# Optimization experiments

Measured on AMD Instinct MI355X. Metric: run time of the kernel, lower is better.

The kernel has to match this reference:

```python
import jax, jax.numpy as jnp
import numpy as np

# SREChead (single level, width=0.25): stem 1x1 (128->64) + two 3x3 convs (64->64),
# each Conv->BN(eval, folded into scale/shift)->SiLU, then 1x1 reg (4ch) and obj (1ch)
# heads, followed by YOLOX-style grid decode.
B, C_IN, HGT, WID = 64, 128, 80, 80
C_H = 64            # int(256 * 0.25)
STRIDE = 32


def _conv(x, w):
    # NCHW conv, stride 1, SAME padding (pad=(k-1)//2 as in BaseConv)
    return jax.lax.conv_general_dilated(
        x, w, window_strides=(1, 1), padding='SAME',
        dimension_numbers=('NCHW', 'OIHW', 'NCHW'))


def _bn_silu(y, scale, shift):
    # eval-mode BatchNorm folded to per-channel affine, then SiLU
    return jax.nn.silu(y * scale[None, :, None, None] + shift[None, :, None, None])


def setup_inputs() -> dict:
    key = jax.random.key(0)
    ks = jax.random.split(key, 12)

    def w(k, o, i, kh, kw, s=0.05):
        return jax.random.normal(k, (o, i, kh, kw), jnp.float32) * s

    def bn(k, c):
        k1, k2 = jax.random.split(k)
        scale = 1.0 + 0.1 * jax.random.normal(k1, (c,), jnp.float32)
        shift = 0.05 * jax.random.normal(k2, (c,), jnp.float32)
        return scale, shift

    stem_scale, stem_shift = bn(ks[2], C_H)
    c1_scale, c1_shift = bn(ks[4], C_H)
    c2_scale, c2_shift = bn(ks[6], C_H)
    return {
        'x': jax.random.normal(ks[0], (B, C_IN, HGT, WID), jnp.float32),
        'stem_w': w(ks[1], C_H, C_IN, 1, 1),
        'stem_scale': stem_scale, 'stem_shift': stem_shift,
        'c1_w': w(ks[3], C_H, C_H, 3, 3),
        'c1_scale': c1_scale, 'c1_shift': c1_shift,
        'c2_w': w(ks[5], C_H, C_H, 3, 3),
        'c2_scale': c2_scale, 'c2_shift': c2_shift,
        'reg_w': w(ks[7], 4, C_H, 1, 1),
        'reg_b': jnp.zeros((4,), jnp.float32),
        'obj_w': w(ks[8], 1, C_H, 1, 1),
        'obj_b': jnp.zeros((1,), jnp.float32),
    }


def reference(x, stem_w, stem_scale, stem_shift,
              c1_w, c1_scale, c1_shift,
              c2_w, c2_scale, c2_shift,
              reg_w, reg_b, obj_w, obj_b):
    f = _bn_silu(_conv(x, stem_w), stem_scale, stem_shift)       # [B,64,H,W]
    f = _bn_silu(_conv(f, c1_w), c1_scale, c1_shift)
    f = _bn_silu(_conv(f, c2_w), c2_scale, c2_shift)
    reg = _conv(f, reg_w) + reg_b[None, :, None, None]           # [B,4,H,W]
    obj = jax.nn.sigmoid(_conv(f, obj_w) + obj_b[None, :, None, None])  # [B,1,H,W]
    out = jnp.concatenate([reg, obj], axis=1)                    # [B,5,H,W]
    out = out.reshape(out.shape[0], 5, HGT * WID).transpose(0, 2, 1)  # [B,HW,5]
    # YOLOX decode: xy = (pred_xy + grid) * stride, wh = exp(pred_wh) * stride
    yv, xv = jnp.meshgrid(jnp.arange(HGT), jnp.arange(WID), indexing='ij')
    grid = jnp.stack([xv, yv], -1).reshape(1, HGT * WID, 2).astype(out.dtype)
    xy = (out[..., :2] + grid) * STRIDE
    wh = jnp.exp(out[..., 2:4]) * STRIDE
    return jnp.concatenate([xy, wh, out[..., 4:5]], axis=-1)     # [B,HW,5]
```

## Files before the change

### kernel.cpp

```cpp
#include <hip/hip_runtime.h>
#include <cstdint>


typedef short short8 __attribute__((ext_vector_type(8)));
typedef float floatx4 __attribute__((ext_vector_type(4)));
typedef float fx4 __attribute__((ext_vector_type(4)));
typedef unsigned short us4 __attribute__((ext_vector_type(4)));

#define NPIX 6400
#define CGS 3952
#define SGS 1024

static __device__ __forceinline__ unsigned short f2bf(float f) {
    unsigned u = __builtin_bit_cast(unsigned, f);
    u += 0x7fffu + ((u >> 16) & 1u);
    return (unsigned short)(u >> 16);
}

static __device__ __forceinline__ float silu_(float v) {
    return v / (1.0f + __expf(-v));
}

__global__ __launch_bounds__(256) void rearr_w_kernel(
    const float* __restrict__ ws_, const float* __restrict__ w1,
    const float* __restrict__ w2,
    unsigned short* __restrict__ wS, unsigned short* __restrict__ wB1,
    unsigned short* __restrict__ wB2) {
    int idx = blockIdx.x * 256 + threadIdx.x;
    if (idx < 8192) {
        int e = idx;
        int j = e & 7, lane = (e >> 3) & 63, ct = (e >> 9) & 3, kb = e >> 11;
        int co = ct * 16 + (lane & 15);
        int ci = kb * 32 + ((lane >> 4) * 8) + j;
        wS[e] = f2bf(ws_[co * 128 + ci]);
        return;
    }
    idx -= 8192;
    const float* src = (idx < 36864) ? w1 : w2;
    unsigned short* dst = (idx < 36864) ? wB1 : wB2;
    int e = (idx < 36864) ? idx : idx - 36864;
    int j = e & 7, lane = (e >> 3) & 63, ct = (e >> 9) & 3, kb = e >> 11;
    int co = ct * 16 + (lane & 15);
    int k = kb * 32 + ((lane >> 4) * 8) + j;
    int ci = k & 63, tap = k >> 6;
    dst[e] = f2bf(src[(co * 64 + ci) * 9 + tap]);
}

__global__ __launch_bounds__(256) void stem_kernel(
    const float* __restrict__ x, const unsigned short* __restrict__ wS,
    const float* __restrict__ scale, const float* __restrict__ shift,
    unsigned short* __restrict__ f1) {
    __shared__ __align__(16) unsigned short xt[16 * SGS];
    int b = blockIdx.y;
    int tid = threadIdx.x;
    int pbase = blockIdx.x * 128;
    int lane = tid & 63, wv = tid >> 6;
    int l15 = lane & 15, q = lane >> 4;

    #pragma unroll
    for (int k = 0; k < 8; ++k) {
        int item = k * 256 + tid;
        int g = item >> 7, px = item & 127;
        const float* xp = x + ((size_t)b * 128 + g * 8) * NPIX + pbase + px;
        unsigned short tmp[8];
        #pragma unroll
        for (int j = 0; j < 8; ++j) tmp[j] = f2bf(xp[j * NPIX]);
        *(short8*)(xt + g * SGS + px * 8) = *(const short8*)tmp;
    }

    float sc[4][4], sh[4][4];
    #pragma unroll
    for (int ct = 0; ct < 4; ++ct)
        #pragma unroll
        for (int r = 0; r < 4; ++r) {
            sc[ct][r] = scale[ct * 16 + q * 4 + r];
            sh[ct][r] = shift[ct * 16 + q * 4 + r];
        }

    __syncthreads();

    floatx4 acc[4][2];
    floatx4 zf = {0.0f, 0.0f, 0.0f, 0.0f};
    #pragma unroll
    for (int ct = 0; ct < 4; ++ct)
        #pragma unroll
        for (int t = 0; t < 2; ++t) acc[ct][t] = zf;

    #pragma unroll
    for (int kb = 0; kb < 4; ++kb) {
        short8 wf[4];
        #pragma unroll
        for (int ct = 0; ct < 4; ++ct)
            wf[ct] = *(const short8*)(wS + ((kb * 4 + ct) * 64 + lane) * 8);
        short8 xf[2];
        #pragma unroll
        for (int t = 0; t < 2; ++t) {
            int px = (wv * 2 + t) * 16 + l15;
            xf[t] = *(const short8*)(xt + (kb * 4 + q) * SGS + px * 8);
        }
        #pragma unroll
        for (int ct = 0; ct < 4; ++ct)
            #pragma unroll
            for (int t = 0; t < 2; ++t)
                acc[ct][t] = __builtin_amdgcn_mfma_f32_16x16x32_bf16(
                    wf[ct], xf[t], acc[ct][t], 0, 0, 0);
    }

    #pragma unroll
    for (int t = 0; t < 2; ++t) {
        int pg = pbase + (wv * 2 + t) * 16 + l15;
        unsigned short* dst = f1 + ((size_t)b * NPIX + pg) * 64;
        #pragma unroll
        for (int ct = 0; ct < 4; ++ct) {
            us4 v;
            #pragma unroll
            for (int r = 0; r < 4; ++r)
                v[r] = f2bf(silu_(acc[ct][t][r] * sc[ct][r] + sh[ct][r]));
            *(us4*)(dst + ct * 16 + q * 4) = v;
        }
    }
}

static __device__ __forceinline__ void conv_core(
    const unsigned short* __restrict__ fin, const unsigned short* __restrict__ wB,
    unsigned short* tile, floatx4* acc, int b, int y0,
    int tid, int lane, int wv, int l15, int q) {
    const unsigned short* fb = fin + (size_t)b * NPIX * 64;
    #pragma unroll
    for (int i = 0; i < 16; ++i) {
        int cid = i * 256 + tid;
        if (cid < 3936) {
            int pixL = cid >> 3, chunk = cid & 7;
            int r = pixL / 82, c = pixL - r * 82;
            int gy = y0 - 1 + r, gx = c - 1;
            short8 v = {};
            if ((unsigned)gy < 80u && (unsigned)gx < 80u)
                v = *(const short8*)(fb + (size_t)(gy * 80 + gx) * 64 + chunk * 8);
            *(short8*)(tile + chunk * CGS + pixL * 8) = v;
        }
    }

    __syncthreads();

    floatx4 zf = {0.0f, 0.0f, 0.0f, 0.0f};
    #pragma unroll
    for (int pt = 0; pt < 20; ++pt) acc[pt] = zf;

    #pragma unroll
    for (int trow = 0; trow < 3; ++trow) {
        short8 wrow[6];
        #pragma unroll
        for (int i = 0; i < 6; ++i)
            wrow[i] = *(const short8*)(wB + (((trow * 6 + i) * 4 + wv) * 64 + lane) * 8);
        const int dy = trow - 1;
        #pragma unroll
        for (int tc = 0; tc < 3; ++tc) {
            const int dx = tc - 1;
            #pragma unroll
            for (int half = 0; half < 2; ++half) {
                short8 w8 = wrow[tc * 2 + half];
                #pragma unroll
                for (int pt = 0; pt < 20; ++pt) {
                    const int r_o = pt / 5, c_o = (pt % 5) * 16;
                    int pix = (r_o + 1 + dy) * 82 + c_o + l15 + 1 + dx;
                    short8 b8 = *(const short8*)(tile + (half * 4 + q) * CGS + pix * 8);
                    acc[pt] = __builtin_amdgcn_mfma_f32_16x16x32_bf16(
                        w8, b8, acc[pt], 0, 0, 0);
                }
            }
        }
    }
}

__global__ __launch_bounds__(256) void conv3_kernel(
    const unsigned short* __restrict__ fin, const unsigned short* __restrict__ wB,
    const float* __restrict__ scale, const float* __restrict__ shift,
    unsigned short* __restrict__ fout) {
    __shared__ __align__(16) unsigned short tile[8 * CGS];
    int b = blockIdx.y, y0 = blockIdx.x * 4;
    int tid = threadIdx.x;
    int lane = tid & 63, wv = tid >> 6;
    int l15 = lane & 15, q = lane >> 4;

    floatx4 acc[20];
    conv_core(fin, wB, tile, acc, b, y0, tid, lane, wv, l15, q);

    float sc4[4], sh4[4];
    #pragma unroll
    for (int r = 0; r < 4; ++r) {
        sc4[r] = scale[wv * 16 + q * 4 + r];
        sh4[r] = shift[wv * 16 + q * 4 + r];
    }
    #pragma unroll
    for (int pt = 0; pt < 20; ++pt) {
        const int r_o = pt / 5, c_o = (pt % 5) * 16;
        int pg = (y0 + r_o) * 80 + c_o + l15;
        us4 v;
        #pragma unroll
        for (int r = 0; r < 4; ++r)
            v[r] = f2bf(silu_(acc[pt][r] * sc4[r] + sh4[r]));
        *(us4*)(fout + ((size_t)b * NPIX + pg) * 64 + wv * 16 + q * 4) = v;
    }
}

__global__ __launch_bounds__(256) void conv_head_kernel(
    const unsigned short* __restrict__ fin, const unsigned short* __restrict__ wB,
    const float* __restrict__ scale, const float* __restrict__ shift,
    const float* __restrict__ reg_w, const float* __restrict__ reg_b,
    const float* __restrict__ obj_w, const float* __restrict__ obj_b,
    float* __restrict__ out) {
    __shared__ __align__(16) unsigned short tile[8 * CGS];
    int b = blockIdx.y, y0 = blockIdx.x * 4;
    int tid = threadIdx.x;
    int lane = tid & 63, wv = tid >> 6;
    int l15 = lane & 15, q = lane >> 4;

    floatx4 acc[20];
    conv_core(fin, wB, tile, acc, b, y0, tid, lane, wv, l15, q);

    __syncthreads();

    float sc4[4], sh4[4];
    #pragma unroll
    for (int r = 0; r < 4; ++r) {
        sc4[r] = scale[wv * 16 + q * 4 + r];
        sh4[r] = shift[wv * 16 + q * 4 + r];
    }
    int gco = wv * 2 + (q >> 1);
    #pragma unroll
    for (int pt = 0; pt < 20; ++pt) {
        const int r_o = pt / 5, c_o = (pt % 5) * 16;
        int pix = r_o * 80 + c_o + l15;
        us4 v;
        #pragma unroll
        for (int r = 0; r < 4; ++r)
            v[r] = f2bf(silu_(acc[pt][r] * sc4[r] + sh4[r]));
        *(us4*)(tile + gco * CGS + pix * 8 + (q & 1) * 4) = v;
    }

    short8 hbf[2];
    #pragma unroll
    for (int kb2 = 0; kb2 < 2; ++kb2) {
        int k0 = kb2 * 32 + q * 8;
        short8 f = {};
        if (l15 < 4) {
            #pragma unroll
            for (int j = 0; j < 8; ++j) f[j] = (short)f2bf(reg_w[l15 * 64 + k0 + j]);
        } else if (l15 == 4) {
            #pragma unroll
            for (int j = 0; j < 8; ++j) f[j] = (short)f2bf(obj_w[k0 + j]);
        }
        hbf[kb2] = f;
    }

    __syncthreads();

    floatx4 zf = {0.0f, 0.0f, 0.0f, 0.0f};
    floatx4 acc5[5];
    #pragma unroll
    for (int t = 0; t < 5; ++t) acc5[t] = zf;
    #pragma unroll
    for (int t = 0; t < 5; ++t) {
        int mt = wv * 5 + t;
        #pragma unroll
        for (int kb2 = 0; kb2 < 2; ++kb2) {
            int pix = mt * 16 + l15;
            short8 a = *(const short8*)(tile + (kb2 * 4 + q) * CGS + pix * 8);
            acc5[t] = __builtin_amdgcn_mfma_f32_16x16x32_bf16(
                a, hbf[kb2], acc5[t], 0, 0, 0);
        }
    }

    float bias = 0.0f;
    if (l15 < 4) bias = reg_b[l15];
    else if (l15 == 4) bias = obj_b[0];

    #pragma unroll
    for (int t = 0; t < 5; ++t) {
        int mt = wv * 5 + t;
        #pragma unroll
        for (int r = 0; r < 4; ++r) {
            int pixL = mt * 16 + q * 4 + r;
            if (l15 < 5) {
                float v = acc5[t][r] + bias;
                float gx = (float)(pixL % 80);
                float gy = (float)(y0 + pixL / 80);
                float o;
                if (l15 == 0)      o = (v + gx) * 32.0f;
                else if (l15 == 1) o = (v + gy) * 32.0f;
                else if (l15 < 4)  o = __expf(v) * 32.0f;
                else               o = 1.0f / (1.0f + __expf(-v));
                out[((size_t)b * NPIX + y0 * 80 + pixL) * 5 + l15] = o;
            }
        }
    }
}

extern "C" void kernel_launch(void* const* d_in, const int* in_sizes, int n_in,
                              void* d_out, int out_size, void* d_ws, size_t ws_size,
                              hipStream_t stream) {
    const float* x          = (const float*)d_in[0];
    const float* stem_w     = (const float*)d_in[1];
    const float* stem_scale = (const float*)d_in[2];
    const float* stem_shift = (const float*)d_in[3];
    const float* c1_w       = (const float*)d_in[4];
    const float* c1_scale   = (const float*)d_in[5];
    const float* c1_shift   = (const float*)d_in[6];
    const float* c2_w       = (const float*)d_in[7];
    const float* c2_scale   = (const float*)d_in[8];
    const float* c2_shift   = (const float*)d_in[9];
    const float* reg_w      = (const float*)d_in[10];
    const float* reg_b      = (const float*)d_in[11];
    const float* obj_w      = (const float*)d_in[12];
    const float* obj_b      = (const float*)d_in[13];
    float* out = (float*)d_out;

    const size_t needed = ((size_t)8192 + 73728 + 2 * (size_t)64 * NPIX * 64) * 2;
    if (ws_size < needed) return;

    unsigned short* ws  = (unsigned short*)d_ws;
    unsigned short* wS  = ws;
    unsigned short* wB1 = ws + 8192;
    unsigned short* wB2 = wB1 + 36864;
    unsigned short* f1  = wB2 + 36864;
    unsigned short* f2  = f1 + (size_t)64 * NPIX * 64;

    rearr_w_kernel<<<320, 256, 0, stream>>>(stem_w, c1_w, c2_w, wS, wB1, wB2);
    stem_kernel<<<dim3(50, 64), 256, 0, stream>>>(x, wS, stem_scale, stem_shift, f1);
    conv3_kernel<<<dim3(20, 64), 256, 0, stream>>>(f1, wB1, c1_scale, c1_shift, f2);
    conv_head_kernel<<<dim3(20, 64), 256, 0, stream>>>(f2, wB2, c2_scale, c2_shift,
                                                       reg_w, reg_b, obj_w, obj_b, out);
}
```

Measured before the change: 498.9 us.

## Restructure 3x3 conv waves per output row, halve LDS tile, coalesce stem loads

The 3x3 conv core now stages the input in two 32-channel halves, which shrinks the LDS tile. Each wave now computes one output row for all 64 output channels instead of 16 channels over 20 pixel tiles. Each B-fragment read from LDS therefore feeds four MFMAs, cutting LDS read traffic, and the conv kernels request 3 blocks per CU. The stem kernel now loads fp32 input with coalesced float4 reads into a padded LDS buffer and converts to bf16 when building fragments, rather than doing strided scalar global loads. The costs are an extra barrier per half, more accumulator registers per wave, and weight fragments reloaded per tap.

Result: faster. 445.9 us (-10.6%).

```diff
diff --git a/kernel.cpp b/kernel.cpp
--- a/kernel.cpp
+++ b/kernel.cpp
@@ -8,8 +8,8 @@
 typedef unsigned short us4 __attribute__((ext_vector_type(4)));
 
 #define NPIX 6400
-#define CGS 3952
-#define SGS 1024
+#define CGS  3952
+#define CGS2 2576
 
 static __device__ __forceinline__ unsigned short f2bf(float f) {
     unsigned u = __builtin_bit_cast(unsigned, f);
@@ -50,24 +50,13 @@
     const float* __restrict__ x, const unsigned short* __restrict__ wS,
     const float* __restrict__ scale, const float* __restrict__ shift,
     unsigned short* __restrict__ f1) {
-    __shared__ __align__(16) unsigned short xt[16 * SGS];
+    __shared__ __align__(16) float xs[64 * 129];
     int b = blockIdx.y;
     int tid = threadIdx.x;
     int pbase = blockIdx.x * 128;
     int lane = tid & 63, wv = tid >> 6;
     int l15 = lane & 15, q = lane >> 4;
 
-    #pragma unroll
-    for (int k = 0; k < 8; ++k) {
-        int item = k * 256 + tid;
-        int g = item >> 7, px = item & 127;
-        const float* xp = x + ((size_t)b * 128 + g * 8) * NPIX + pbase + px;
-        unsigned short tmp[8];
-        #pragma unroll
-        for (int j = 0; j < 8; ++j) tmp[j] = f2bf(xp[j * NPIX]);
-        *(short8*)(xt + g * SGS + px * 8) = *(const short8*)tmp;
-    }
-
     float sc[4][4], sh[4][4];
     #pragma unroll
     for (int ct = 0; ct < 4; ++ct)
@@ -77,8 +66,6 @@
             sh[ct][r] = shift[ct * 16 + q * 4 + r];
         }
 
-    __syncthreads();
-
     floatx4 acc[4][2];
     floatx4 zf = {0.0f, 0.0f, 0.0f, 0.0f};
     #pragma unroll
@@ -87,23 +74,42 @@
         for (int t = 0; t < 2; ++t) acc[ct][t] = zf;
 
     #pragma unroll
-    for (int kb = 0; kb < 4; ++kb) {
-        short8 wf[4];
-        #pragma unroll
-        for (int ct = 0; ct < 4; ++ct)
-            wf[ct] = *(const short8*)(wS + ((kb * 4 + ct) * 64 + lane) * 8);
-        short8 xf[2];
-        #pragma unroll
-        for (int t = 0; t < 2; ++t) {
-            int px = (wv * 2 + t) * 16 + l15;
-            xf[t] = *(const short8*)(xt + (kb * 4 + q) * SGS + px * 8);
-        }
-        #pragma unroll
-        for (int ct = 0; ct < 4; ++ct)
-            #pragma unroll
-            for (int t = 0; t < 2; ++t)
-                acc[ct][t] = __builtin_amdgcn_mfma_f32_16x16x32_bf16(
-                    wf[ct], xf[t], acc[ct][t], 0, 0, 0);
+    for (int p = 0; p < 2; ++p) {
+        if (p) __syncthreads();
+        #pragma unroll
+        for (int i = 0; i < 8; ++i) {
+            int c = i * 256 + tid;
+            int row = c >> 5, seg = c & 31;
+            fx4 v = *(const fx4*)(
+                x + ((size_t)(b * 128 + p * 64 + row)) * NPIX + pbase + seg * 4);
+            *(fx4*)(xs + row * 129 + seg * 4) = v;
+        }
+        __syncthreads();
+
+        #pragma unroll
+        for (int kk = 0; kk < 2; ++kk) {
+            int kb = p * 2 + kk;
+            short8 wf[4];
+            #pragma unroll
+            for (int ct = 0; ct < 4; ++ct)
+                wf[ct] = *(const short8*)(wS + ((kb * 4 + ct) * 64 + lane) * 8);
+            short8 xf[2];
+            #pragma unroll
+            for (int t = 0; t < 2; ++t) {
+                int px = (wv * 2 + t) * 16 + l15;
+                const float* src = xs + (kk * 32 + q * 8) * 129 + px;
+                unsigned short tmp[8];
+                #pragma unroll
+                for (int j = 0; j < 8; ++j) tmp[j] = f2bf(src[j * 129]);
+                xf[t] = *(const short8*)tmp;
+            }
+            #pragma unroll
+            for (int ct = 0; ct < 4; ++ct)
+                #pragma unroll
+                for (int t = 0; t < 2; ++t)
+                    acc[ct][t] = __builtin_amdgcn_mfma_f32_16x16x32_bf16(
+                        wf[ct], xf[t], acc[ct][t], 0, 0, 0);
+        }
     }
 
     #pragma unroll
@@ -123,119 +129,132 @@
 
 static __device__ __forceinline__ void conv_core(
     const unsigned short* __restrict__ fin, const unsigned short* __restrict__ wB,
-    unsigned short* tile, floatx4* acc, int b, int y0,
+    unsigned short* tile, floatx4 (*acc)[5], int b, int y0,
     int tid, int lane, int wv, int l15, int q) {
     const unsigned short* fb = fin + (size_t)b * NPIX * 64;
-    #pragma unroll
-    for (int i = 0; i < 16; ++i) {
-        int cid = i * 256 + tid;
-        if (cid < 3936) {
-            int pixL = cid >> 3, chunk = cid & 7;
-            int r = pixL / 82, c = pixL - r * 82;
-            int gy = y0 - 1 + r, gx = c - 1;
-            short8 v = {};
-            if ((unsigned)gy < 80u && (unsigned)gx < 80u)
-                v = *(const short8*)(fb + (size_t)(gy * 80 + gx) * 64 + chunk * 8);
-            *(short8*)(tile + chunk * CGS + pixL * 8) = v;
-        }
-    }
-
-    __syncthreads();
-
     floatx4 zf = {0.0f, 0.0f, 0.0f, 0.0f};
     #pragma unroll
-    for (int pt = 0; pt < 20; ++pt) acc[pt] = zf;
-
-    #pragma unroll
-    for (int trow = 0; trow < 3; ++trow) {
-        short8 wrow[6];
-        #pragma unroll
-        for (int i = 0; i < 6; ++i)
-            wrow[i] = *(const short8*)(wB + (((trow * 6 + i) * 4 + wv) * 64 + lane) * 8);
-        const int dy = trow - 1;
-        #pragma unroll
-        for (int tc = 0; tc < 3; ++tc) {
-            const int dx = tc - 1;
-            #pragma unroll
-            for (int half = 0; half < 2; ++half) {
-                short8 w8 = wrow[tc * 2 + half];
+    for (int c4 = 0; c4 < 4; ++c4)
+        #pragma unroll
+        for (int pt = 0; pt < 5; ++pt) acc[c4][pt] = zf;
+
+    #pragma unroll
+    for (int half = 0; half < 2; ++half) {
+        if (half) __syncthreads();
+        #pragma unroll
+        for (int i = 0; i < 8; ++i) {
+            int cid = i * 256 + tid;
+            if (cid < 1968) {
+                int pixL = cid >> 2, g = cid & 3;
+                int r = pixL / 82, c = pixL - r * 82;
+                int gy = y0 - 1 + r, gx = c - 1;
+                short8 v = {};
+                if ((unsigned)gy < 80u && (unsigned)gx < 80u)
+                    v = *(const short8*)(
+                        fb + (size_t)(gy * 80 + gx) * 64 + half * 32 + g * 8);
+                *(short8*)(tile + g * CGS + pixL * 8) = v;
+            }
+        }
+        __syncthreads();
+
+        #pragma unroll
+        for (int trow = 0; trow < 3; ++trow) {
+            const int dy = trow - 1;
+            #pragma unroll
+            for (int tc = 0; tc < 3; ++tc) {
+                const int dx = tc - 1;
+                const int kb = (trow * 3 + tc) * 2 + half;
+                short8 w4[4];
                 #pragma unroll
-                for (int pt = 0; pt < 20; ++pt) {
-                    const int r_o = pt / 5, c_o = (pt % 5) * 16;
-                    int pix = (r_o + 1 + dy) * 82 + c_o + l15 + 1 + dx;
-                    short8 b8 = *(const short8*)(tile + (half * 4 + q) * CGS + pix * 8);
-                    acc[pt] = __builtin_amdgcn_mfma_f32_16x16x32_bf16(
-                        w8, b8, acc[pt], 0, 0, 0);
+                for (int c4 = 0; c4 < 4; ++c4)
+                    w4[c4] = *(const short8*)(wB + ((kb * 4 + c4) * 64 + lane) * 8);
+                #pragma unroll
+                for (int pt = 0; pt < 5; ++pt) {
+                    int pix = (wv + 1 + dy) * 82 + pt * 16 + l15 + 1 + dx;
+                    short8 b8 = *(const short8*)(tile + q * CGS + pix * 8);
+                    #pragma unroll
+                    for (int c4 = 0; c4 < 4; ++c4)
+                        acc[c4][pt] = __builtin_amdgcn_mfma_f32_16x16x32_bf16(
+                            w4[c4], b8, acc[c4][pt], 0, 0, 0);
                 }
             }
         }
     }
 }
 
-__global__ __launch_bounds__(256) void conv3_kernel(
+__global__ __launch_bounds__(256, 3) void conv3_kernel(
     const unsigned short* __restrict__ fin, const unsigned short* __restrict__ wB,
     const float* __restrict__ scale, const float* __restrict__ shift,
     unsigned short* __restrict__ fout) {
-    __shared__ __align__(16) unsigned short tile[8 * CGS];
+    __shared__ __align__(16) unsigned short tile[8 * CGS2];
     int b = blockIdx.y, y0 = blockIdx.x * 4;
     int tid = threadIdx.x;
     int lane = tid & 63, wv = tid >> 6;
     int l15 = lane & 15, q = lane >> 4;
 
-    floatx4 acc[20];
+    floatx4 acc[4][5];
     conv_core(fin, wB, tile, acc, b, y0, tid, lane, wv, l15, q);
 
-    float sc4[4], sh4[4];
-    #pragma unroll
-    for (int r = 0; r < 4; ++r) {
-        sc4[r] = scale[wv * 16 + q * 4 + r];
-        sh4[r] = shift[wv * 16 + q * 4 + r];
-    }
-    #pragma unroll
-    for (int pt = 0; pt < 20; ++pt) {
-        const int r_o = pt / 5, c_o = (pt % 5) * 16;
-        int pg = (y0 + r_o) * 80 + c_o + l15;
-        us4 v;
-        #pragma unroll
-        for (int r = 0; r < 4; ++r)
-            v[r] = f2bf(silu_(acc[pt][r] * sc4[r] + sh4[r]));
-        *(us4*)(fout + ((size_t)b * NPIX + pg) * 64 + wv * 16 + q * 4) = v;
-    }
-}
-
-__global__ __launch_bounds__(256) void conv_head_kernel(
+    float sc4[4][4], sh4[4][4];
+    #pragma unroll
+    for (int c4 = 0; c4 < 4; ++c4)
+        #pragma unroll
+        for (int r = 0; r < 4; ++r) {
+            sc4[c4][r] = scale[c4 * 16 + q * 4 + r];
+            sh4[c4][r] = shift[c4 * 16 + q * 4 + r];
+        }
+    #pragma unroll
+    for (int pt = 0; pt < 5; ++pt) {
+        int pg = (y0 + wv) * 80 + pt * 16 + l15;
+        unsigned short* dst = fout + ((size_t)b * NPIX + pg) * 64;
+        #pragma unroll
+        for (int c4 = 0; c4 < 4; ++c4) {
+            us4 v;
+            #pragma unroll
+            for (int r = 0; r < 4; ++r)
+                v[r] = f2bf(silu_(acc[c4][pt][r] * sc4[c4][r] + sh4[c4][r]));
+            *(us4*)(dst + c4 * 16 + q * 4) = v;
+        }
+    }
+}
+
+__global__ __launch_bounds__(256, 3) void conv_head_kernel(
     const unsigned short* __restrict__ fin, const unsigned short* __restrict__ wB,
     const float* __restrict__ scale, const float* __restrict__ shift,
     const float* __restrict__ reg_w, const float* __restrict__ reg_b,
     const float* __restrict__ obj_w, const float* __restrict__ obj_b,
     float* __restrict__ out) {
-    __shared__ __align__(16) unsigned short tile[8 * CGS];
+    __shared__ __align__(16) unsigned short tile[8 * CGS2];
     int b = blockIdx.y, y0 = blockIdx.x * 4;
     int tid = threadIdx.x;
     int lane = tid & 63, wv = tid >> 6;
     int l15 = lane & 15, q = lane >> 4;
 
-    floatx4 acc[20];
+    floatx4 acc[4][5];
     conv_core(fin, wB, tile, acc, b, y0, tid, lane, wv, l15, q);
 
     __syncthreads();
 
-    float sc4[4], sh4[4];
-    #pragma unroll
-    for (int r = 0; r < 4; ++r) {
-        sc4[r] = scale[wv * 16 + q * 4 + r];
-        sh4[r] = shift[wv * 16 + q * 4 + r];
-    }
-    int gco = wv * 2 + (q >> 1);
-    #pragma unroll
-    for (int pt = 0; pt < 20; ++pt) {
-        const int r_o = pt / 5, c_o = (pt % 5) * 16;
-        int pix = r_o * 80 + c_o + l15;
-        us4 v;
-        #pragma unroll
-        for (int r = 0; r < 4; ++r)
-            v[r] = f2bf(silu_(acc[pt][r] * sc4[r] + sh4[r]));
-        *(us4*)(tile + gco * CGS + pix * 8 + (q & 1) * 4) = v;
+    float sc4[4][4], sh4[4][4];
+    #pragma unroll
+    for (int c4 = 0; c4 < 4; ++c4)
+        #pragma unroll
+        for (int r = 0; r < 4; ++r) {
+            sc4[c4][r] = scale[c4 * 16 + q * 4 + r];
+            sh4[c4][r] = shift[c4 * 16 + q * 4 + r];
+        }
+    #pragma unroll
+    for (int pt = 0; pt < 5; ++pt) {
+        int pix = wv * 80 + pt * 16 + l15;
+        #pragma unroll
+        for (int c4 = 0; c4 < 4; ++c4) {
+            int gco = c4 * 2 + (q >> 1);
+            us4 v;
+            #pragma unroll
+            for (int r = 0; r < 4; ++r)
+                v[r] = f2bf(silu_(acc[c4][pt][r] * sc4[c4][r] + sh4[c4][r]));
+            *(us4*)(tile + gco * CGS2 + pix * 8 + (q & 1) * 4) = v;
+        }
     }
 
     short8 hbf[2];
@@ -262,10 +281,10 @@
     #pragma unroll
     for (int t = 0; t < 5; ++t) {
         int mt = wv * 5 + t;
+        int pix = mt * 16 + l15;
         #pragma unroll
         for (int kb2 = 0; kb2 < 2; ++kb2) {
-            int pix = mt * 16 + l15;
-            short8 a = *(const short8*)(tile + (kb2 * 4 + q) * CGS + pix * 8);
+            short8 a = *(const short8*)(tile + (kb2 * 4 + q) * CGS2 + pix * 8);
             acc5[t] = __builtin_amdgcn_mfma_f32_16x16x32_bf16(
                 a, hbf[kb2], acc5[t], 0, 0, 0);
         }
```
